# Kernel tuning notes

Hardware: AMD Instinct MI355X
Metric: run time of the kernel (lower is better)

Reference implementation:

```python
import jax, jax.numpy as jnp
import numpy as np

N = 128   # n_features == out_dim (required by the Christoffel permutes)
H = 256   # MLP hidden width of forward_func
B = 16    # batch size (state_batch is [2B, N])
EPS_G = 1e-4
EPS_DG = 1e-6
EPS_V = 1e-6


def setup_inputs() -> dict:
    key = jax.random.key(0)
    ks = jax.random.split(key, 6)
    return {
        "t": jax.random.uniform(ks[0], (), dtype=jnp.float32),
        "state_batch": jax.random.normal(ks[1], (2 * B, N), dtype=jnp.float32) * 0.1,
        "x0_batch": jax.random.normal(ks[2], (B, N), dtype=jnp.float32),
        "x1_batch": jax.random.normal(ks[3], (B, N), dtype=jnp.float32),
        "W1": jax.random.normal(ks[4], (N, H), dtype=jnp.float32) / np.float32(np.sqrt(N)),
        "b1": jnp.zeros((H,), dtype=jnp.float32),
        "W2": jax.random.normal(ks[5], (H, N), dtype=jnp.float32) / np.float32(np.sqrt(H)),
        "b2": jnp.zeros((N,), dtype=jnp.float32),
    }


def reference(t, state_batch, x0_batch, x1_batch, W1, b1, W2, b2):
    def f(x):  # forward_func, per-sample: [N] -> [N]
        return jnp.tanh(x @ W1 + b1) @ W2 + b2

    def metric(x):  # G(x) = J J^T + 1e-4 I, per-sample: [N] -> [N, N]
        J = jax.jacrev(f)(x)                      # [N, N], matches per-output grad loop
        return J @ J.T + EPS_G * jnp.eye(N, dtype=x.dtype)

    deviation, dev_velocity = jnp.split(state_batch, 2, axis=0)  # each [B, N]
    window = 4.0 * t * (1.0 - t)
    # x along the perturbed straight path
    x = x0_batch + t * (x1_batch - x0_batch) + window * deviation  # [B, N]

    # dG[b, i, j, k] = dG_ij/dx_k -- replaces the out_dim^2 autograd.grad loop
    dG = jax.vmap(jax.jacfwd(metric))(x)  # [B, N, N, N]
    nrm = jnp.sqrt(jnp.sum(dG * dG, axis=(1, 2, 3), keepdims=True))
    dG = dG / (nrm + EPS_DG)

    # Christoffel-like symbols
    Gamma = 0.5 * (dG + jnp.transpose(dG, (0, 2, 1, 3)) - jnp.transpose(dG, (0, 3, 1, 2)))
    a = -jnp.einsum('bijk,bj,bk->bi', Gamma, dev_velocity, dev_velocity)
    a = a / (jnp.linalg.norm(dev_velocity, axis=1, keepdims=True) + EPS_V)

    restoration = -0.1 * deviation
    return jnp.concatenate([dev_velocity, a + restoration], axis=0)  # [2B, N]
```

## Files before the change

kernel.cpp:

```cpp
#include <hip/hip_runtime.h>
#include <math.h>


static constexpr int OFF_W2T  = 0;
static constexpr int OFF_S    = 32768;
static constexpr int OFF_Q    = 98304;
static constexpr int OFF_D    = 163840;
static constexpr int OFF_C    = 167936;
static constexpr int OFF_UV   = 172032;
static constexpr int OFF_AV   = 176128;
static constexpr int OFF_VN   = 180224;
static constexpr int OFF_SUM  = 180240;
static constexpr int OFF_CNT  = 180256;
static constexpr int OFF_PT   = 180272;
static constexpr int OFF_PN   = OFF_PT + 16 * 32768;

__global__ __launch_bounds__(256) void k_stage1(const float* __restrict__ tptr,
                                                const float* __restrict__ state,
                                                const float* __restrict__ x0,
                                                const float* __restrict__ x1,
                                                const float* __restrict__ W1,
                                                const float* __restrict__ b1,
                                                const float* __restrict__ W2,
                                                float* __restrict__ ws,
                                                float* __restrict__ out) {
    __shared__ __align__(16) float smem[2 * 32 * 34];
    int blk = blockIdx.x;
    int tid = threadIdx.x;

    if (blk < 64) {
        float* Ai = smem;
        float* Aj = smem + 1088;
        int m0 = (blk >> 3) * 32, n0 = (blk & 7) * 32;
        int lx = tid & 31, lr = tid >> 5;
        int tx = tid & 15, ty = tid >> 4;
        float a00 = 0, a01 = 0, a10 = 0, a11 = 0;
        for (int kc = 0; kc < 128; kc += 32) {
            #pragma unroll
            for (int i = 0; i < 4; ++i) {
                int k = lr + 8 * i;
                Ai[k * 34 + lx] = W1[(kc + k) * 256 + m0 + lx];
                Aj[k * 34 + lx] = W1[(kc + k) * 256 + n0 + lx];
            }
            __syncthreads();
            #pragma unroll
            for (int k = 0; k < 32; ++k) {
                float2 a = *(const float2*)&Ai[k * 34 + 2 * ty];
                float2 b = *(const float2*)&Aj[k * 34 + 2 * tx];
                a00 += a.x * b.x; a01 += a.x * b.y;
                a10 += a.y * b.x; a11 += a.y * b.y;
            }
            __syncthreads();
        }
        float* S = ws + OFF_S;
        int m = m0 + 2 * ty, n = n0 + 2 * tx;
        S[m * 256 + n]           = a00;
        S[m * 256 + n + 1]       = a01;
        S[(m + 1) * 256 + n]     = a10;
        S[(m + 1) * 256 + n + 1] = a11;
    } else if (blk < 128) {
        float* Xi = smem;
        float* Xj = smem + 1088;
        int bq = blk - 64;
        int m0 = (bq >> 3) * 32, n0 = (bq & 7) * 32;
        int lx = tid & 31, lr = tid >> 5;
        int tx = tid & 15, ty = tid >> 4;
        float a00 = 0, a01 = 0, a10 = 0, a11 = 0;
        for (int kc = 0; kc < 128; kc += 32) {
            #pragma unroll
            for (int i = 0; i < 4; ++i) {
                Xi[lx * 34 + lr + 8 * i] = W2[(m0 + lr + 8 * i) * 128 + kc + lx];
                Xj[lx * 34 + lr + 8 * i] = W2[(n0 + lr + 8 * i) * 128 + kc + lx];
            }
            __syncthreads();
            #pragma unroll
            for (int k = 0; k < 32; ++k) {
                float2 a = *(const float2*)&Xi[k * 34 + 2 * ty];
                float2 b = *(const float2*)&Xj[k * 34 + 2 * tx];
                a00 += a.x * b.x; a01 += a.x * b.y;
                a10 += a.y * b.x; a11 += a.y * b.y;
            }
            __syncthreads();
        }
        float* Q = ws + OFF_Q;
        int m = m0 + 2 * ty, n = n0 + 2 * tx;
        Q[m * 256 + n]           = a00;
        Q[m * 256 + n + 1]       = a01;
        Q[(m + 1) * 256 + n]     = a10;
        Q[(m + 1) * 256 + n + 1] = a11;
    } else if (blk < 160) {
        float* tile = smem;
        int b2 = blk - 128;
        int c0 = (b2 & 3) * 32, r0 = (b2 >> 2) * 32;
        int tx = tid & 31, ty = tid >> 5;
        #pragma unroll
        for (int i = 0; i < 32; i += 8)
            tile[(ty + i) * 33 + tx] = W2[(r0 + ty + i) * 128 + c0 + tx];
        __syncthreads();
        float* W2T = ws + OFF_W2T;
        #pragma unroll
        for (int i = 0; i < 32; i += 8)
            W2T[(c0 + ty + i) * 256 + r0 + tx] = tile[tx * 33 + ty + i];
    } else {
        int b = blk - 160;
        float* xs  = smem;
        float* vs  = smem + 128;
        float* red = smem + 256;
        float t = tptr[0];
        float w = 4.f * t * (1.f - t);
        if (tid == 0) {
            ws[OFF_SUM + b] = 0.f;
            ((int*)(ws + OFF_CNT))[b] = 0;
        }
        if (tid < 128) {
            float dev = state[b * 128 + tid];
            float v   = state[(16 + b) * 128 + tid];
            float xv  = x0[b * 128 + tid] + t * (x1[b * 128 + tid] - x0[b * 128 + tid]) + w * dev;
            xs[tid] = xv;
            vs[tid] = v;
            out[b * 128 + tid] = v;
            red[tid] = v * v;
        }
        __syncthreads();
        for (int s = 64; s > 0; s >>= 1) {
            if (tid < s) red[tid] += red[tid + s];
            __syncthreads();
        }
        if (tid == 0) ws[OFF_VN + b] = sqrtf(red[0]);

        int m = tid;
        float h = b1[m], uvm = 0.f;
        #pragma unroll 8
        for (int k = 0; k < 128; ++k) {
            float wv = W1[k * 256 + m];
            h   += xs[k] * wv;
            uvm += vs[k] * wv;
        }
        float z  = tanhf(h);
        float dd = 1.f - z * z;
        float cc = -2.f * z * dd;
        const float4* w2r = (const float4*)&W2[m * 128];
        const float4* vs4 = (const float4*)vs;
        float avm = 0.f;
        #pragma unroll 8
        for (int j4 = 0; j4 < 32; ++j4) {
            float4 ww = w2r[j4];
            float4 vv = vs4[j4];
            avm += ww.x * vv.x + ww.y * vv.y + ww.z * vv.z + ww.w * vv.w;
        }
        ws[OFF_D  + b * 256 + m] = dd;
        ws[OFF_C  + b * 256 + m] = cc;
        ws[OFF_UV + b * 256 + m] = uvm;
        ws[OFF_AV + b * 256 + m] = avm;
    }
}

__global__ __launch_bounds__(256) void k_pmat3(const float* __restrict__ Smat,
                                               const float* __restrict__ dall,
                                               const float* __restrict__ W2,
                                               float* __restrict__ PT,
                                               float* __restrict__ Pn) {
    __shared__ __align__(16) float ST[32 * 36];
    __shared__ __align__(16) float YT[32 * 68];
    int b = blockIdx.z, mt = blockIdx.y, jt = blockIdx.x;
    int m0 = mt * 32, j0 = jt * 64;
    const float* dvec = dall + b * 256;
    int tid = threadIdx.x;
    int n = tid >> 3, c4 = (tid & 7) * 4;
    int ty = tid >> 5, tx = tid & 31;
    float acc[4][2] = {};
    for (int nc = 0; nc < 256; nc += 32) {
        *(float4*)&ST[n * 36 + c4] = *(const float4*)&Smat[(nc + n) * 256 + m0 + c4];
        float dn = dvec[nc + n];
        #pragma unroll
        for (int i = 0; i < 2; ++i) {
            int col = c4 + 32 * i;
            float4 wv = *(const float4*)&W2[(nc + n) * 128 + j0 + col];
            wv.x *= dn; wv.y *= dn; wv.z *= dn; wv.w *= dn;
            *(float4*)&YT[n * 68 + col] = wv;
        }
        __syncthreads();
        #pragma unroll 8
        for (int k = 0; k < 32; ++k) {
            float4 a  = *(const float4*)&ST[k * 36 + 4 * ty];
            float2 bb = *(const float2*)&YT[k * 68 + 2 * tx];
            acc[0][0] += a.x * bb.x; acc[0][1] += a.x * bb.y;
            acc[1][0] += a.y * bb.x; acc[1][1] += a.y * bb.y;
            acc[2][0] += a.z * bb.x; acc[2][1] += a.z * bb.y;
            acc[3][0] += a.w * bb.x; acc[3][1] += a.w * bb.y;
        }
        __syncthreads();
    }
    float* ptb = PT + b * 32768;
    float* pnb = Pn + b * 32768;
    #pragma unroll
    for (int jj = 0; jj < 2; ++jj) {
        float4 v = make_float4(acc[0][jj], acc[1][jj], acc[2][jj], acc[3][jj]);
        *(float4*)&ptb[(j0 + 2 * tx + jj) * 256 + m0 + 4 * ty] = v;
    }
    #pragma unroll
    for (int ii = 0; ii < 4; ++ii) {
        float2 v = make_float2(acc[ii][0], acc[ii][1]);
        *(float2*)&pnb[(m0 + 4 * ty + ii) * 128 + j0 + 2 * tx] = v;
    }
}

__global__ __launch_bounds__(256, 3) void k_fnorm6(const float* __restrict__ state,
                                                   const float* __restrict__ W2,
                                                   float* __restrict__ ws,
                                                   float* __restrict__ out) {
    __shared__ __align__(16) float lds[12544];
    int blk = blockIdx.x;
    int tid = threadIdx.x;
    int* cnt = (int*)(ws + OFF_CNT);

    if (blk < 16) {
        int b = blk;
        const float* ptb = ws + OFF_PT + b * 32768;
        const float* pnb = ws + OFF_PN + b * 32768;
        float* vs   = lds;
        float* g1   = lds + 128;
        float* g2   = lds + 384;
        float* red  = lds + 640;
        float* snrm = lds + 900;
        if (tid < 128) vs[tid] = state[(16 + b) * 128 + tid];
        __syncthreads();

        int m = tid;
        float pv = 0.f;
        #pragma unroll 8
        for (int j = 0; j < 128; ++j)
            pv += ptb[j * 256 + m] * vs[j];
        float cc  = ws[OFF_C  + b * 256 + m];
        float uvm = ws[OFF_UV + b * 256 + m];
        float avm = ws[OFF_AV + b * 256 + m];
        g1[m] = cc * pv  * uvm;
        g2[m] = cc * avm * uvm;
        __syncthreads();

        int i = tid & 127, half = tid >> 7;
        int mmlo = half * 128;
        float raw = 0.f;
        #pragma unroll 8
        for (int mm = mmlo; mm < mmlo + 128; ++mm)
            raw += W2[mm * 128 + i] * g1[mm] + pnb[mm * 128 + i] * g2[mm];
        red[tid] = raw;
        __syncthreads();

        if (tid == 0) {
            while (atomicAdd(&cnt[b], 0) < 36) __builtin_amdgcn_s_sleep(2);
            __threadfence();
            float tot = atomicAdd(&ws[OFF_SUM + b], 0.0f);
            snrm[0] = sqrtf(fmaxf(2.f * tot, 0.f));
        }
        __syncthreads();
        if (tid < 128) {
            float rawt = red[tid] + red[tid + 128];
            float vn = ws[OFF_VN + b];
            float a  = -0.5f * rawt / ((snrm[0] + 1e-6f) * (vn + 1e-6f));
            out[(16 + b) * 128 + tid] = a - 0.1f * state[b * 128 + tid];
        }
        return;
    }

    int q   = blk - 16;
    int idx = q >> 4;
    int b   = q & 15;
    int tj = 0;
    while ((tj + 1) * (tj + 2) / 2 <= idx) ++tj;
    int ti = idx - tj * (tj + 1) / 2;
    int mi0 = ti * 32, mj0 = tj * 32;
    float* PiT = lds;
    float* PjT = lds + 2048;
    float* WiT = lds + 4096;
    float* WjT = lds + 6144;
    const float* ptb = ws + OFF_PT + b * 32768;
    const float* W2T = ws + OFF_W2T;
    const float* Smat = ws + OFF_S;
    const float* Qmat = ws + OFF_Q;
    int jr = tid >> 3, jc4 = (tid & 7) * 4;
    int w = tid >> 6, s = tid & 63;
    int ty = s >> 3, tx = s & 7;
    float r[4][4] = {}, f[4][4] = {}, g[4][4] = {};
    #pragma unroll
    for (int rr = 0; rr < 2; ++rr) {
        #pragma unroll
        for (int it = 0; it < 2; ++it) {
            int l = jr + 32 * it;
            int j = 32 * (l >> 4) + 16 * rr + (l & 15);
            *(float4*)&PiT[l * 32 + jc4] = *(const float4*)&ptb[j * 256 + mi0 + jc4];
            *(float4*)&PjT[l * 32 + jc4] = *(const float4*)&ptb[j * 256 + mj0 + jc4];
            *(float4*)&WiT[l * 32 + jc4] = *(const float4*)&W2T[j * 256 + mi0 + jc4];
            *(float4*)&WjT[l * 32 + jc4] = *(const float4*)&W2T[j * 256 + mj0 + jc4];
        }
        __syncthreads();
        #pragma unroll 4
        for (int jj = 0; jj < 16; ++jj) {
            int l = 16 * w + jj;
            float4 pi4 = *(const float4*)&PiT[l * 32 + 4 * ty];
            float4 pj4 = *(const float4*)&PjT[l * 32 + 4 * tx];
            float4 wi4 = *(const float4*)&WiT[l * 32 + 4 * ty];
            float4 wj4 = *(const float4*)&WjT[l * 32 + 4 * tx];
            float pi[4] = {pi4.x, pi4.y, pi4.z, pi4.w};
            float pj[4] = {pj4.x, pj4.y, pj4.z, pj4.w};
            float wi[4] = {wi4.x, wi4.y, wi4.z, wi4.w};
            float wj[4] = {wj4.x, wj4.y, wj4.z, wj4.w};
            #pragma unroll
            for (int ii = 0; ii < 4; ++ii)
                #pragma unroll
                for (int kk = 0; kk < 4; ++kk) {
                    r[ii][kk] += pi[ii] * pj[kk];
                    f[ii][kk] += pi[ii] * wj[kk];
                    g[ii][kk] += pj[kk] * wi[ii];
                }
        }
        __syncthreads();
    }
    {
        float* scr = lds;
        int base = tid * 49;
        #pragma unroll
        for (int ii = 0; ii < 4; ++ii)
            #pragma unroll
            for (int kk = 0; kk < 4; ++kk) {
                scr[base + ii * 4 + kk]      = r[ii][kk];
                scr[base + 16 + ii * 4 + kk] = f[ii][kk];
                scr[base + 32 + ii * 4 + kk] = g[ii][kk];
            }
    }
    __syncthreads();
    if (tid < 64) {
        const float* scr = lds;
        float tr[16], tf[16], tg[16];
        #pragma unroll
        for (int k = 0; k < 16; ++k) {
            tr[k] = scr[tid * 49 + k]           + scr[(tid + 64) * 49 + k]
                  + scr[(tid + 128) * 49 + k]   + scr[(tid + 192) * 49 + k];
            tf[k] = scr[tid * 49 + 16 + k]      + scr[(tid + 64) * 49 + 16 + k]
                  + scr[(tid + 128) * 49 + 16 + k] + scr[(tid + 192) * 49 + 16 + k];
            tg[k] = scr[tid * 49 + 32 + k]      + scr[(tid + 64) * 49 + 32 + k]
                  + scr[(tid + 128) * 49 + 32 + k] + scr[(tid + 192) * 49 + 32 + k];
        }
        const float* cb = ws + OFF_C + b * 256;
        int mi = mi0 + 4 * (tid >> 3), mj = mj0 + 4 * (tid & 7);
        float4 ce4 = *(const float4*)&cb[mj];
        float ce[4] = {ce4.x, ce4.y, ce4.z, ce4.w};
        float sum = 0.f;
        #pragma unroll
        for (int ii = 0; ii < 4; ++ii) {
            float ci = cb[mi + ii];
            float4 S4 = *(const float4*)&Smat[(mi + ii) * 256 + mj];
            float4 Q4 = *(const float4*)&Qmat[(mi + ii) * 256 + mj];
            float Sv[4] = {S4.x, S4.y, S4.z, S4.w};
            float Qv[4] = {Q4.x, Q4.y, Q4.z, Q4.w};
            #pragma unroll
            for (int kk = 0; kk < 4; ++kk)
                sum += ci * ce[kk] * Sv[kk] * (Qv[kk] * tr[ii * 4 + kk] + tf[ii * 4 + kk] * tg[ii * 4 + kk]);
        }
        if (ti < tj) sum *= 2.f;
        #pragma unroll
        for (int off = 32; off > 0; off >>= 1)
            sum += __shfl_down(sum, off);
        if (tid == 0) {
            atomicAdd(&ws[OFF_SUM + b], sum);
            __threadfence();
            atomicAdd(&cnt[b], 1);
        }
    }
}

extern "C" void kernel_launch(void* const* d_in, const int* in_sizes, int n_in,
                              void* d_out, int out_size, void* d_ws, size_t ws_size,
                              hipStream_t stream) {
    (void)in_sizes; (void)n_in; (void)out_size; (void)ws_size;
    const float* t     = (const float*)d_in[0];
    const float* state = (const float*)d_in[1];
    const float* x0    = (const float*)d_in[2];
    const float* x1    = (const float*)d_in[3];
    const float* W1    = (const float*)d_in[4];
    const float* b1    = (const float*)d_in[5];
    const float* W2    = (const float*)d_in[6];
    float* out = (float*)d_out;
    float* ws  = (float*)d_ws;

    k_stage1<<<176, 256, 0, stream>>>(t, state, x0, x1, W1, b1, W2, ws, out);
    k_pmat3<<<dim3(2, 8, 16), 256, 0, stream>>>(ws + OFF_S, ws + OFF_D, W2,
                                                ws + OFF_PT, ws + OFF_PN);
    k_fnorm6<<<592, 256, 0, stream>>>(state, W2, ws, out);
}
```

Baseline: 115.0 us.

## Fuse three kernels into one persistent launch with inter-block flag dependencies

Merges the stage1, pmat3 and fnorm6 kernels into a single 976-block launch. Producer blocks signal completion with magic-number flags in workspace, and consumer blocks spin-wait on only the flags they depend on, which replaces the kernel boundaries with fine-grained dataflow. Some stage1 roles now process two tiles per block to cut the producer block count, and the final reduction reads one partial set from registers. This removes launch gaps and full-grid barriers, but relies on all producers being scheduled ahead of spinning consumers; stale magic values left in workspace from a previous call could also release waiters early.

```diff
diff --git a/kernel.cpp b/kernel.cpp
--- a/kernel.cpp
+++ b/kernel.cpp
@@ -12,10 +12,27 @@
 static constexpr int OFF_VN   = 180224;
 static constexpr int OFF_SUM  = 180240;
 static constexpr int OFF_CNT  = 180256;
-static constexpr int OFF_PT   = 180272;
+static constexpr int IFL_S    = 180272;
+static constexpr int IFL_Q    = IFL_S + 128;
+static constexpr int IFL_T    = IFL_Q + 64;
+static constexpr int IFL_PREP = IFL_T + 32;
+static constexpr int IFL_P    = IFL_PREP + 32;
+static constexpr int OFF_PT   = IFL_P + 512;
 static constexpr int OFF_PN   = OFF_PT + 16 * 32768;
 
-__global__ __launch_bounds__(256) void k_stage1(const float* __restrict__ tptr,
+#define MAG1 0x1357ACE5
+#define MAG2 0x2468BD1B
+
+__device__ __forceinline__ void set_flag2(int* f) {
+    atomicExch(f, MAG1);
+    atomicExch(f + 1, MAG2);
+}
+__device__ __forceinline__ void wait_flag2(int* f) {
+    while (atomicAdd(f, 0) != MAG1) __builtin_amdgcn_s_sleep(8);
+    while (atomicAdd(f + 1, 0) != MAG2) __builtin_amdgcn_s_sleep(8);
+}
+
+__global__ __launch_bounds__(256, 4) void k_all(const float* __restrict__ tptr,
                                                 const float* __restrict__ state,
                                                 const float* __restrict__ x0,
                                                 const float* __restrict__ x1,
@@ -24,13 +41,15 @@
                                                 const float* __restrict__ W2,
                                                 float* __restrict__ ws,
                                                 float* __restrict__ out) {
-    __shared__ __align__(16) float smem[2 * 32 * 34];
+    __shared__ __align__(16) float lds[9408];
     int blk = blockIdx.x;
     int tid = threadIdx.x;
+    int* flg = (int*)ws;
+    int* cnt = flg + OFF_CNT;
 
     if (blk < 64) {
-        float* Ai = smem;
-        float* Aj = smem + 1088;
+        float* Ai = lds;
+        float* Aj = lds + 1088;
         int m0 = (blk >> 3) * 32, n0 = (blk & 7) * 32;
         int lx = tid & 31, lr = tid >> 5;
         int tx = tid & 15, ty = tid >> 4;
@@ -58,59 +77,71 @@
         S[m * 256 + n + 1]       = a01;
         S[(m + 1) * 256 + n]     = a10;
         S[(m + 1) * 256 + n + 1] = a11;
+        __syncthreads();
+        if (tid == 0) { __threadfence(); set_flag2(flg + IFL_S + 2 * blk); }
+    } else if (blk < 96) {
+        int bqq = blk - 64;
+        for (int hh = 0; hh < 2; ++hh) {
+            int bq = bqq + 32 * hh;
+            float* Xi = lds;
+            float* Xj = lds + 1088;
+            int m0 = (bq >> 3) * 32, n0 = (bq & 7) * 32;
+            int lx = tid & 31, lr = tid >> 5;
+            int tx = tid & 15, ty = tid >> 4;
+            float a00 = 0, a01 = 0, a10 = 0, a11 = 0;
+            for (int kc = 0; kc < 128; kc += 32) {
+                #pragma unroll
+                for (int i = 0; i < 4; ++i) {
+                    Xi[lx * 34 + lr + 8 * i] = W2[(m0 + lr + 8 * i) * 128 + kc + lx];
+                    Xj[lx * 34 + lr + 8 * i] = W2[(n0 + lr + 8 * i) * 128 + kc + lx];
+                }
+                __syncthreads();
+                #pragma unroll
+                for (int k = 0; k < 32; ++k) {
+                    float2 a = *(const float2*)&Xi[k * 34 + 2 * ty];
+                    float2 b = *(const float2*)&Xj[k * 34 + 2 * tx];
+                    a00 += a.x * b.x; a01 += a.x * b.y;
+                    a10 += a.y * b.x; a11 += a.y * b.y;
+                }
+                __syncthreads();
+            }
+            float* Q = ws + OFF_Q;
+            int m = m0 + 2 * ty, n = n0 + 2 * tx;
+            Q[m * 256 + n]           = a00;
+            Q[m * 256 + n + 1]       = a01;
+            Q[(m + 1) * 256 + n]     = a10;
+            Q[(m + 1) * 256 + n + 1] = a11;
+            __syncthreads();
+        }
+        if (tid == 0) { __threadfence(); set_flag2(flg + IFL_Q + 2 * bqq); }
+    } else if (blk < 112) {
+        int bt = blk - 96;
+        for (int hh = 0; hh < 2; ++hh) {
+            int b2 = bt + 16 * hh;
+            float* tile = lds;
+            int c0 = (b2 & 3) * 32, r0 = (b2 >> 2) * 32;
+            int tx = tid & 31, ty = tid >> 5;
+            #pragma unroll
+            for (int i = 0; i < 32; i += 8)
+                tile[(ty + i) * 33 + tx] = W2[(r0 + ty + i) * 128 + c0 + tx];
+            __syncthreads();
+            float* W2T = ws + OFF_W2T;
+            #pragma unroll
+            for (int i = 0; i < 32; i += 8)
+                W2T[(c0 + ty + i) * 256 + r0 + tx] = tile[tx * 33 + ty + i];
+            __syncthreads();
+        }
+        if (tid == 0) { __threadfence(); set_flag2(flg + IFL_T + 2 * bt); }
     } else if (blk < 128) {
-        float* Xi = smem;
-        float* Xj = smem + 1088;
-        int bq = blk - 64;
-        int m0 = (bq >> 3) * 32, n0 = (bq & 7) * 32;
-        int lx = tid & 31, lr = tid >> 5;
-        int tx = tid & 15, ty = tid >> 4;
-        float a00 = 0, a01 = 0, a10 = 0, a11 = 0;
-        for (int kc = 0; kc < 128; kc += 32) {
-            #pragma unroll
-            for (int i = 0; i < 4; ++i) {
-                Xi[lx * 34 + lr + 8 * i] = W2[(m0 + lr + 8 * i) * 128 + kc + lx];
-                Xj[lx * 34 + lr + 8 * i] = W2[(n0 + lr + 8 * i) * 128 + kc + lx];
-            }
-            __syncthreads();
-            #pragma unroll
-            for (int k = 0; k < 32; ++k) {
-                float2 a = *(const float2*)&Xi[k * 34 + 2 * ty];
-                float2 b = *(const float2*)&Xj[k * 34 + 2 * tx];
-                a00 += a.x * b.x; a01 += a.x * b.y;
-                a10 += a.y * b.x; a11 += a.y * b.y;
-            }
-            __syncthreads();
-        }
-        float* Q = ws + OFF_Q;
-        int m = m0 + 2 * ty, n = n0 + 2 * tx;
-        Q[m * 256 + n]           = a00;
-        Q[m * 256 + n + 1]       = a01;
-        Q[(m + 1) * 256 + n]     = a10;
-        Q[(m + 1) * 256 + n + 1] = a11;
-    } else if (blk < 160) {
-        float* tile = smem;
-        int b2 = blk - 128;
-        int c0 = (b2 & 3) * 32, r0 = (b2 >> 2) * 32;
-        int tx = tid & 31, ty = tid >> 5;
-        #pragma unroll
-        for (int i = 0; i < 32; i += 8)
-            tile[(ty + i) * 33 + tx] = W2[(r0 + ty + i) * 128 + c0 + tx];
-        __syncthreads();
-        float* W2T = ws + OFF_W2T;
-        #pragma unroll
-        for (int i = 0; i < 32; i += 8)
-            W2T[(c0 + ty + i) * 256 + r0 + tx] = tile[tx * 33 + ty + i];
-    } else {
-        int b = blk - 160;
-        float* xs  = smem;
-        float* vs  = smem + 128;
-        float* red = smem + 256;
+        int b = blk - 112;
+        float* xs  = lds;
+        float* vs  = lds + 128;
+        float* red = lds + 256;
         float t = tptr[0];
         float w = 4.f * t * (1.f - t);
         if (tid == 0) {
             ws[OFF_SUM + b] = 0.f;
-            ((int*)(ws + OFF_CNT))[b] = 0;
+            cnt[b] = 0;
         }
         if (tid < 128) {
             float dev = state[b * 128 + tid];
@@ -152,70 +183,185 @@
         ws[OFF_C  + b * 256 + m] = cc;
         ws[OFF_UV + b * 256 + m] = uvm;
         ws[OFF_AV + b * 256 + m] = avm;
-    }
-}
-
-__global__ __launch_bounds__(256) void k_pmat3(const float* __restrict__ Smat,
-                                               const float* __restrict__ dall,
-                                               const float* __restrict__ W2,
-                                               float* __restrict__ PT,
-                                               float* __restrict__ Pn) {
-    __shared__ __align__(16) float ST[32 * 36];
-    __shared__ __align__(16) float YT[32 * 68];
-    int b = blockIdx.z, mt = blockIdx.y, jt = blockIdx.x;
-    int m0 = mt * 32, j0 = jt * 64;
-    const float* dvec = dall + b * 256;
-    int tid = threadIdx.x;
-    int n = tid >> 3, c4 = (tid & 7) * 4;
-    int ty = tid >> 5, tx = tid & 31;
-    float acc[4][2] = {};
-    for (int nc = 0; nc < 256; nc += 32) {
-        *(float4*)&ST[n * 36 + c4] = *(const float4*)&Smat[(nc + n) * 256 + m0 + c4];
-        float dn = dvec[nc + n];
+        __syncthreads();
+        if (tid == 0) { __threadfence(); set_flag2(flg + IFL_PREP + 2 * b); }
+    } else if (blk < 384) {
+        int q = blk - 128;
+        int b = q >> 4, rem = q & 15;
+        int mt = rem >> 1, jt = rem & 1;
+        if (tid < 64) wait_flag2(flg + IFL_S + 2 * tid);
+        else if (tid == 64) wait_flag2(flg + IFL_PREP + 2 * b);
+        __syncthreads();
+        __threadfence();
+
+        float* ST = lds;
+        float* YT = lds + 1152;
+        const float* Smat = ws + OFF_S;
+        const float* dvec = ws + OFF_D + b * 256;
+        int m0 = mt * 32, j0 = jt * 64;
+        int n = tid >> 3, c4 = (tid & 7) * 4;
+        int ty = tid >> 5, tx = tid & 31;
+        float acc[4][2] = {};
+        for (int nc = 0; nc < 256; nc += 32) {
+            *(float4*)&ST[n * 36 + c4] = *(const float4*)&Smat[(nc + n) * 256 + m0 + c4];
+            float dn = dvec[nc + n];
+            #pragma unroll
+            for (int i = 0; i < 2; ++i) {
+                int col = c4 + 32 * i;
+                float4 wv = *(const float4*)&W2[(nc + n) * 128 + j0 + col];
+                wv.x *= dn; wv.y *= dn; wv.z *= dn; wv.w *= dn;
+                *(float4*)&YT[n * 68 + col] = wv;
+            }
+            __syncthreads();
+            #pragma unroll 8
+            for (int k = 0; k < 32; ++k) {
+                float4 a  = *(const float4*)&ST[k * 36 + 4 * ty];
+                float2 bb = *(const float2*)&YT[k * 68 + 2 * tx];
+                acc[0][0] += a.x * bb.x; acc[0][1] += a.x * bb.y;
+                acc[1][0] += a.y * bb.x; acc[1][1] += a.y * bb.y;
+                acc[2][0] += a.z * bb.x; acc[2][1] += a.z * bb.y;
+                acc[3][0] += a.w * bb.x; acc[3][1] += a.w * bb.y;
+            }
+            __syncthreads();
+        }
+        float* ptb = ws + OFF_PT + b * 32768;
+        float* pnb = ws + OFF_PN + b * 32768;
         #pragma unroll
-        for (int i = 0; i < 2; ++i) {
-            int col = c4 + 32 * i;
-            float4 wv = *(const float4*)&W2[(nc + n) * 128 + j0 + col];
-            wv.x *= dn; wv.y *= dn; wv.z *= dn; wv.w *= dn;
-            *(float4*)&YT[n * 68 + col] = wv;
-        }
-        __syncthreads();
-        #pragma unroll 8
-        for (int k = 0; k < 32; ++k) {
-            float4 a  = *(const float4*)&ST[k * 36 + 4 * ty];
-            float2 bb = *(const float2*)&YT[k * 68 + 2 * tx];
-            acc[0][0] += a.x * bb.x; acc[0][1] += a.x * bb.y;
-            acc[1][0] += a.y * bb.x; acc[1][1] += a.y * bb.y;
-            acc[2][0] += a.z * bb.x; acc[2][1] += a.z * bb.y;
-            acc[3][0] += a.w * bb.x; acc[3][1] += a.w * bb.y;
-        }
-        __syncthreads();
-    }
-    float* ptb = PT + b * 32768;
-    float* pnb = Pn + b * 32768;
-    #pragma unroll
-    for (int jj = 0; jj < 2; ++jj) {
-        float4 v = make_float4(acc[0][jj], acc[1][jj], acc[2][jj], acc[3][jj]);
-        *(float4*)&ptb[(j0 + 2 * tx + jj) * 256 + m0 + 4 * ty] = v;
-    }
-    #pragma unroll
-    for (int ii = 0; ii < 4; ++ii) {
-        float2 v = make_float2(acc[ii][0], acc[ii][1]);
-        *(float2*)&pnb[(m0 + 4 * ty + ii) * 128 + j0 + 2 * tx] = v;
-    }
-}
-
-__global__ __launch_bounds__(256, 3) void k_fnorm6(const float* __restrict__ state,
-                                                   const float* __restrict__ W2,
-                                                   float* __restrict__ ws,
-                                                   float* __restrict__ out) {
-    __shared__ __align__(16) float lds[12544];
-    int blk = blockIdx.x;
-    int tid = threadIdx.x;
-    int* cnt = (int*)(ws + OFF_CNT);
-
-    if (blk < 16) {
-        int b = blk;
+        for (int jj = 0; jj < 2; ++jj) {
+            float4 v = make_float4(acc[0][jj], acc[1][jj], acc[2][jj], acc[3][jj]);
+            *(float4*)&ptb[(j0 + 2 * tx + jj) * 256 + m0 + 4 * ty] = v;
+        }
+        #pragma unroll
+        for (int ii = 0; ii < 4; ++ii) {
+            float2 v = make_float2(acc[ii][0], acc[ii][1]);
+            *(float2*)&pnb[(m0 + 4 * ty + ii) * 128 + j0 + 2 * tx] = v;
+        }
+        __syncthreads();
+        if (tid == 0) { __threadfence(); set_flag2(flg + IFL_P + 2 * q); }
+    } else if (blk < 960) {
+        int q = blk - 384;
+        int idx = q >> 4;
+        int b   = q & 15;
+        if (tid < 16) wait_flag2(flg + IFL_P + 2 * (16 * b + tid));
+        else if (tid < 48) wait_flag2(flg + IFL_Q + 2 * (tid - 16));
+        else if (tid < 64) wait_flag2(flg + IFL_T + 2 * (tid - 48));
+        __syncthreads();
+        __threadfence();
+
+        int tj = 0;
+        while ((tj + 1) * (tj + 2) / 2 <= idx) ++tj;
+        int ti = idx - tj * (tj + 1) / 2;
+        int mi0 = ti * 32, mj0 = tj * 32;
+        float* PiT = lds;
+        float* PjT = lds + 2048;
+        float* WiT = lds + 4096;
+        float* WjT = lds + 6144;
+        const float* ptb  = ws + OFF_PT + b * 32768;
+        const float* W2T  = ws + OFF_W2T;
+        const float* Smat = ws + OFF_S;
+        const float* Qmat = ws + OFF_Q;
+        int jr = tid >> 3, jc4 = (tid & 7) * 4;
+        int w = tid >> 6, s = tid & 63;
+        int ty = s >> 3, tx = s & 7;
+        float r[4][4] = {}, f[4][4] = {}, g[4][4] = {};
+        #pragma unroll
+        for (int rr = 0; rr < 2; ++rr) {
+            #pragma unroll
+            for (int it = 0; it < 2; ++it) {
+                int l = jr + 32 * it;
+                int j = 32 * (l >> 4) + 16 * rr + (l & 15);
+                *(float4*)&PiT[l * 32 + jc4] = *(const float4*)&ptb[j * 256 + mi0 + jc4];
+                *(float4*)&PjT[l * 32 + jc4] = *(const float4*)&ptb[j * 256 + mj0 + jc4];
+                *(float4*)&WiT[l * 32 + jc4] = *(const float4*)&W2T[j * 256 + mi0 + jc4];
+                *(float4*)&WjT[l * 32 + jc4] = *(const float4*)&W2T[j * 256 + mj0 + jc4];
+            }
+            __syncthreads();
+            #pragma unroll 4
+            for (int jj = 0; jj < 16; ++jj) {
+                int l = 16 * w + jj;
+                float4 pi4 = *(const float4*)&PiT[l * 32 + 4 * ty];
+                float4 pj4 = *(const float4*)&PjT[l * 32 + 4 * tx];
+                float4 wi4 = *(const float4*)&WiT[l * 32 + 4 * ty];
+                float4 wj4 = *(const float4*)&WjT[l * 32 + 4 * tx];
+                float pi[4] = {pi4.x, pi4.y, pi4.z, pi4.w};
+                float pj[4] = {pj4.x, pj4.y, pj4.z, pj4.w};
+                float wi[4] = {wi4.x, wi4.y, wi4.z, wi4.w};
+                float wj[4] = {wj4.x, wj4.y, wj4.z, wj4.w};
+                #pragma unroll
+                for (int ii = 0; ii < 4; ++ii)
+                    #pragma unroll
+                    for (int kk = 0; kk < 4; ++kk) {
+                        r[ii][kk] += pi[ii] * pj[kk];
+                        f[ii][kk] += pi[ii] * wj[kk];
+                        g[ii][kk] += pj[kk] * wi[ii];
+                    }
+            }
+            __syncthreads();
+        }
+        if (w != 0) {
+            float* scr = lds;
+            int base = ((w - 1) * 64 + s) * 49;
+            #pragma unroll
+            for (int ii = 0; ii < 4; ++ii)
+                #pragma unroll
+                for (int kk = 0; kk < 4; ++kk) {
+                    scr[base + ii * 4 + kk]      = r[ii][kk];
+                    scr[base + 16 + ii * 4 + kk] = f[ii][kk];
+                    scr[base + 32 + ii * 4 + kk] = g[ii][kk];
+                }
+        }
+        __syncthreads();
+        if (tid < 64) {
+            float tr[16], tf[16], tg[16];
+            #pragma unroll
+            for (int ii = 0; ii < 4; ++ii)
+                #pragma unroll
+                for (int kk = 0; kk < 4; ++kk) {
+                    tr[ii * 4 + kk] = r[ii][kk];
+                    tf[ii * 4 + kk] = f[ii][kk];
+                    tg[ii * 4 + kk] = g[ii][kk];
+                }
+            for (int ww = 0; ww < 3; ++ww) {
+                const float* sc = lds + (ww * 64 + tid) * 49;
+                #pragma unroll
+                for (int k = 0; k < 16; ++k) {
+                    tr[k] += sc[k];
+                    tf[k] += sc[16 + k];
+                    tg[k] += sc[32 + k];
+                }
+            }
+            const float* cb = ws + OFF_C + b * 256;
+            int mi = mi0 + 4 * (tid >> 3), mj = mj0 + 4 * (tid & 7);
+            float4 ce4 = *(const float4*)&cb[mj];
+            float ce[4] = {ce4.x, ce4.y, ce4.z, ce4.w};
+            float sum = 0.f;
+            #pragma unroll
+            for (int ii = 0; ii < 4; ++ii) {
+                float ci = cb[mi + ii];
+                float4 S4 = *(const float4*)&Smat[(mi + ii) * 256 + mj];
+                float4 Q4 = *(const float4*)&Qmat[(mi + ii) * 256 + mj];
+                float Sv[4] = {S4.x, S4.y, S4.z, S4.w};
+                float Qv[4] = {Q4.x, Q4.y, Q4.z, Q4.w};
+                #pragma unroll
+                for (int kk = 0; kk < 4; ++kk)
+                    sum += ci * ce[kk] * Sv[kk] * (Qv[kk] * tr[ii * 4 + kk] + tf[ii * 4 + kk] * tg[ii * 4 + kk]);
+            }
+            if (ti < tj) sum *= 2.f;
+            #pragma unroll
+            for (int off = 32; off > 0; off >>= 1)
+                sum += __shfl_down(sum, off);
+            if (tid == 0) {
+                atomicAdd(&ws[OFF_SUM + b], sum);
+                __threadfence();
+                atomicAdd(&cnt[b], 1);
+            }
+        }
+    } else {
+        int b = blk - 960;
+        if (tid < 16) wait_flag2(flg + IFL_P + 2 * (16 * b + tid));
+        __syncthreads();
+        __threadfence();
+
         const float* ptb = ws + OFF_PT + b * 32768;
         const float* pnb = ws + OFF_PN + b * 32768;
         float* vs   = lds;
@@ -248,7 +394,7 @@
         __syncthreads();
 
         if (tid == 0) {
-            while (atomicAdd(&cnt[b], 0) < 36) __builtin_amdgcn_s_sleep(2);
+            while (atomicAdd(&cnt[b], 0) < 36) __builtin_amdgcn_s_sleep(8);
             __threadfence();
             float tot = atomicAdd(&ws[OFF_SUM + b], 0.0f);
             snrm[0] = sqrtf(fmaxf(2.f * tot, 0.f));
@@ -259,112 +405,6 @@
             float vn = ws[OFF_VN + b];
             float a  = -0.5f * rawt / ((snrm[0] + 1e-6f) * (vn + 1e-6f));
             out[(16 + b) * 128 + tid] = a - 0.1f * state[b * 128 + tid];
-        }
-        return;
-    }
-
-    int q   = blk - 16;
-    int idx = q >> 4;
-    int b   = q & 15;
-    int tj = 0;
-    while ((tj + 1) * (tj + 2) / 2 <= idx) ++tj;
-    int ti = idx - tj * (tj + 1) / 2;
-    int mi0 = ti * 32, mj0 = tj * 32;
-    float* PiT = lds;
-    float* PjT = lds + 2048;
-    float* WiT = lds + 4096;
-    float* WjT = lds + 6144;
-    const float* ptb = ws + OFF_PT + b * 32768;
-    const float* W2T = ws + OFF_W2T;
-    const float* Smat = ws + OFF_S;
-    const float* Qmat = ws + OFF_Q;
-    int jr = tid >> 3, jc4 = (tid & 7) * 4;
-    int w = tid >> 6, s = tid & 63;
-    int ty = s >> 3, tx = s & 7;
-    float r[4][4] = {}, f[4][4] = {}, g[4][4] = {};
-    #pragma unroll
-    for (int rr = 0; rr < 2; ++rr) {
-        #pragma unroll
-        for (int it = 0; it < 2; ++it) {
-            int l = jr + 32 * it;
-            int j = 32 * (l >> 4) + 16 * rr + (l & 15);
-            *(float4*)&PiT[l * 32 + jc4] = *(const float4*)&ptb[j * 256 + mi0 + jc4];
-            *(float4*)&PjT[l * 32 + jc4] = *(const float4*)&ptb[j * 256 + mj0 + jc4];
-            *(float4*)&WiT[l * 32 + jc4] = *(const float4*)&W2T[j * 256 + mi0 + jc4];
-            *(float4*)&WjT[l * 32 + jc4] = *(const float4*)&W2T[j * 256 + mj0 + jc4];
-        }
-        __syncthreads();
-        #pragma unroll 4
-        for (int jj = 0; jj < 16; ++jj) {
-            int l = 16 * w + jj;
-            float4 pi4 = *(const float4*)&PiT[l * 32 + 4 * ty];
-            float4 pj4 = *(const float4*)&PjT[l * 32 + 4 * tx];
-            float4 wi4 = *(const float4*)&WiT[l * 32 + 4 * ty];
-            float4 wj4 = *(const float4*)&WjT[l * 32 + 4 * tx];
-            float pi[4] = {pi4.x, pi4.y, pi4.z, pi4.w};
-            float pj[4] = {pj4.x, pj4.y, pj4.z, pj4.w};
-            float wi[4] = {wi4.x, wi4.y, wi4.z, wi4.w};
-            float wj[4] = {wj4.x, wj4.y, wj4.z, wj4.w};
-            #pragma unroll
-            for (int ii = 0; ii < 4; ++ii)
-                #pragma unroll
-                for (int kk = 0; kk < 4; ++kk) {
-                    r[ii][kk] += pi[ii] * pj[kk];
-                    f[ii][kk] += pi[ii] * wj[kk];
-                    g[ii][kk] += pj[kk] * wi[ii];
-                }
-        }
-        __syncthreads();
-    }
-    {
-        float* scr = lds;
-        int base = tid * 49;
-        #pragma unroll
-        for (int ii = 0; ii < 4; ++ii)
-            #pragma unroll
-            for (int kk = 0; kk < 4; ++kk) {
-                scr[base + ii * 4 + kk]      = r[ii][kk];
-                scr[base + 16 + ii * 4 + kk] = f[ii][kk];
-                scr[base + 32 + ii * 4 + kk] = g[ii][kk];
-            }
-    }
-    __syncthreads();
-    if (tid < 64) {
-        const float* scr = lds;
-        float tr[16], tf[16], tg[16];
-        #pragma unroll
-        for (int k = 0; k < 16; ++k) {
-            tr[k] = scr[tid * 49 + k]           + scr[(tid + 64) * 49 + k]
-                  + scr[(tid + 128) * 49 + k]   + scr[(tid + 192) * 49 + k];
-            tf[k] = scr[tid * 49 + 16 + k]      + scr[(tid + 64) * 49 + 16 + k]
-                  + scr[(tid + 128) * 49 + 16 + k] + scr[(tid + 192) * 49 + 16 + k];
-            tg[k] = scr[tid * 49 + 32 + k]      + scr[(tid + 64) * 49 + 32 + k]
-                  + scr[(tid + 128) * 49 + 32 + k] + scr[(tid + 192) * 49 + 32 + k];
-        }
-        const float* cb = ws + OFF_C + b * 256;
-        int mi = mi0 + 4 * (tid >> 3), mj = mj0 + 4 * (tid & 7);
-        float4 ce4 = *(const float4*)&cb[mj];
-        float ce[4] = {ce4.x, ce4.y, ce4.z, ce4.w};
-        float sum = 0.f;
-        #pragma unroll
-        for (int ii = 0; ii < 4; ++ii) {
-            float ci = cb[mi + ii];
-            float4 S4 = *(const float4*)&Smat[(mi + ii) * 256 + mj];
-            float4 Q4 = *(const float4*)&Qmat[(mi + ii) * 256 + mj];
-            float Sv[4] = {S4.x, S4.y, S4.z, S4.w};
-            float Qv[4] = {Q4.x, Q4.y, Q4.z, Q4.w};
-            #pragma unroll
-            for (int kk = 0; kk < 4; ++kk)
-                sum += ci * ce[kk] * Sv[kk] * (Qv[kk] * tr[ii * 4 + kk] + tf[ii * 4 + kk] * tg[ii * 4 + kk]);
-        }
-        if (ti < tj) sum *= 2.f;
-        #pragma unroll
-        for (int off = 32; off > 0; off >>= 1)
-            sum += __shfl_down(sum, off);
-        if (tid == 0) {
-            atomicAdd(&ws[OFF_SUM + b], sum);
-            __threadfence();
-            atomicAdd(&cnt[b], 1);
         }
     }
 }
@@ -383,8 +423,5 @@
     float* out = (float*)d_out;
     float* ws  = (float*)d_ws;
 
-    k_stage1<<<176, 256, 0, stream>>>(t, state, x0, x1, W1, b1, W2, ws, out);
-    k_pmat3<<<dim3(2, 8, 16), 256, 0, stream>>>(ws + OFF_S, ws + OFF_D, W2,
-                                                ws + OFF_PT, ws + OFF_PN);
-    k_fnorm6<<<592, 256, 0, stream>>>(state, W2, ws, out);
+    k_all<<<976, 256, 0, stream>>>(t, state, x0, x1, W1, b1, W2, ws, out);
 }
```

Measured after the change: 206.8 us. 79.8% more time.

## Fuse P-matrix GEMM into the norm kernel with per-batch counter handoff

Applied to the files above, without the earlier changes.

Merges the P-matrix GEMM kernel and the norm/output kernel into one launch of 848 blocks. The first 256 blocks compute PT/Pn and signal per-batch completion through a new counter. The norm-tile and final-output blocks spin-wait on that counter instead of relying on a kernel boundary, which removes one launch and lets batches proceed independently. The block order is rearranged so the output blocks come last, and the cross-wave reduction keeps wave 0's partials in registers, which cuts LDS use and allows occupancy 4. The cost is spin-wait deadlock risk if the consumer blocks become resident before the producers, plus sleep/poll overhead.

```diff
diff --git a/kernel.cpp b/kernel.cpp
--- a/kernel.cpp
+++ b/kernel.cpp
@@ -12,7 +12,8 @@
 static constexpr int OFF_VN   = 180224;
 static constexpr int OFF_SUM  = 180240;
 static constexpr int OFF_CNT  = 180256;
-static constexpr int OFF_PT   = 180272;
+static constexpr int OFF_CNT2 = 180272;
+static constexpr int OFF_PT   = 180288;
 static constexpr int OFF_PN   = OFF_PT + 16 * 32768;
 
 __global__ __launch_bounds__(256) void k_stage1(const float* __restrict__ tptr,
@@ -110,7 +111,8 @@
         float w = 4.f * t * (1.f - t);
         if (tid == 0) {
             ws[OFF_SUM + b] = 0.f;
-            ((int*)(ws + OFF_CNT))[b] = 0;
+            ((int*)ws)[OFF_CNT + b]  = 0;
+            ((int*)ws)[OFF_CNT2 + b] = 0;
         }
         if (tid < 128) {
             float dev = state[b * 128 + tid];
@@ -155,67 +157,190 @@
     }
 }
 
-__global__ __launch_bounds__(256) void k_pmat3(const float* __restrict__ Smat,
-                                               const float* __restrict__ dall,
-                                               const float* __restrict__ W2,
-                                               float* __restrict__ PT,
-                                               float* __restrict__ Pn) {
-    __shared__ __align__(16) float ST[32 * 36];
-    __shared__ __align__(16) float YT[32 * 68];
-    int b = blockIdx.z, mt = blockIdx.y, jt = blockIdx.x;
-    int m0 = mt * 32, j0 = jt * 64;
-    const float* dvec = dall + b * 256;
-    int tid = threadIdx.x;
-    int n = tid >> 3, c4 = (tid & 7) * 4;
-    int ty = tid >> 5, tx = tid & 31;
-    float acc[4][2] = {};
-    for (int nc = 0; nc < 256; nc += 32) {
-        *(float4*)&ST[n * 36 + c4] = *(const float4*)&Smat[(nc + n) * 256 + m0 + c4];
-        float dn = dvec[nc + n];
-        #pragma unroll
-        for (int i = 0; i < 2; ++i) {
-            int col = c4 + 32 * i;
-            float4 wv = *(const float4*)&W2[(nc + n) * 128 + j0 + col];
-            wv.x *= dn; wv.y *= dn; wv.z *= dn; wv.w *= dn;
-            *(float4*)&YT[n * 68 + col] = wv;
-        }
-        __syncthreads();
-        #pragma unroll 8
-        for (int k = 0; k < 32; ++k) {
-            float4 a  = *(const float4*)&ST[k * 36 + 4 * ty];
-            float2 bb = *(const float2*)&YT[k * 68 + 2 * tx];
-            acc[0][0] += a.x * bb.x; acc[0][1] += a.x * bb.y;
-            acc[1][0] += a.y * bb.x; acc[1][1] += a.y * bb.y;
-            acc[2][0] += a.z * bb.x; acc[2][1] += a.z * bb.y;
-            acc[3][0] += a.w * bb.x; acc[3][1] += a.w * bb.y;
-        }
-        __syncthreads();
-    }
-    float* ptb = PT + b * 32768;
-    float* pnb = Pn + b * 32768;
-    #pragma unroll
-    for (int jj = 0; jj < 2; ++jj) {
-        float4 v = make_float4(acc[0][jj], acc[1][jj], acc[2][jj], acc[3][jj]);
-        *(float4*)&ptb[(j0 + 2 * tx + jj) * 256 + m0 + 4 * ty] = v;
-    }
-    #pragma unroll
-    for (int ii = 0; ii < 4; ++ii) {
-        float2 v = make_float2(acc[ii][0], acc[ii][1]);
-        *(float2*)&pnb[(m0 + 4 * ty + ii) * 128 + j0 + 2 * tx] = v;
-    }
-}
-
-__global__ __launch_bounds__(256, 3) void k_fnorm6(const float* __restrict__ state,
-                                                   const float* __restrict__ W2,
-                                                   float* __restrict__ ws,
-                                                   float* __restrict__ out) {
-    __shared__ __align__(16) float lds[12544];
+__global__ __launch_bounds__(256, 4) void k_pfuse(const float* __restrict__ state,
+                                                  const float* __restrict__ W2,
+                                                  float* __restrict__ ws,
+                                                  float* __restrict__ out) {
+    __shared__ __align__(16) float lds[9408];
     int blk = blockIdx.x;
     int tid = threadIdx.x;
-    int* cnt = (int*)(ws + OFF_CNT);
-
-    if (blk < 16) {
-        int b = blk;
+    int* cnt  = (int*)ws + OFF_CNT;
+    int* cnt2 = (int*)ws + OFF_CNT2;
+
+    if (blk < 256) {
+        int q = blk;
+        int b = q >> 4, rem = q & 15;
+        int mt = rem >> 1, jt = rem & 1;
+        float* ST = lds;
+        float* YT = lds + 1152;
+        const float* Smat = ws + OFF_S;
+        const float* dvec = ws + OFF_D + b * 256;
+        int m0 = mt * 32, j0 = jt * 64;
+        int n = tid >> 3, c4 = (tid & 7) * 4;
+        int ty = tid >> 5, tx = tid & 31;
+        float acc[4][2] = {};
+        for (int nc = 0; nc < 256; nc += 32) {
+            *(float4*)&ST[n * 36 + c4] = *(const float4*)&Smat[(nc + n) * 256 + m0 + c4];
+            float dn = dvec[nc + n];
+            #pragma unroll
+            for (int i = 0; i < 2; ++i) {
+                int col = c4 + 32 * i;
+                float4 wv = *(const float4*)&W2[(nc + n) * 128 + j0 + col];
+                wv.x *= dn; wv.y *= dn; wv.z *= dn; wv.w *= dn;
+                *(float4*)&YT[n * 68 + col] = wv;
+            }
+            __syncthreads();
+            #pragma unroll 8
+            for (int k = 0; k < 32; ++k) {
+                float4 a  = *(const float4*)&ST[k * 36 + 4 * ty];
+                float2 bb = *(const float2*)&YT[k * 68 + 2 * tx];
+                acc[0][0] += a.x * bb.x; acc[0][1] += a.x * bb.y;
+                acc[1][0] += a.y * bb.x; acc[1][1] += a.y * bb.y;
+                acc[2][0] += a.z * bb.x; acc[2][1] += a.z * bb.y;
+                acc[3][0] += a.w * bb.x; acc[3][1] += a.w * bb.y;
+            }
+            __syncthreads();
+        }
+        float* ptb = ws + OFF_PT + b * 32768;
+        float* pnb = ws + OFF_PN + b * 32768;
+        #pragma unroll
+        for (int jj = 0; jj < 2; ++jj) {
+            float4 v = make_float4(acc[0][jj], acc[1][jj], acc[2][jj], acc[3][jj]);
+            *(float4*)&ptb[(j0 + 2 * tx + jj) * 256 + m0 + 4 * ty] = v;
+        }
+        #pragma unroll
+        for (int ii = 0; ii < 4; ++ii) {
+            float2 v = make_float2(acc[ii][0], acc[ii][1]);
+            *(float2*)&pnb[(m0 + 4 * ty + ii) * 128 + j0 + 2 * tx] = v;
+        }
+        __syncthreads();
+        if (tid == 0) { __threadfence(); atomicAdd(&cnt2[b], 1); }
+    } else if (blk < 832) {
+        int q = blk - 256;
+        int idx = q >> 4;
+        int b   = q & 15;
+        if (tid == 0) {
+            while (atomicAdd(&cnt2[b], 0) < 16) __builtin_amdgcn_s_sleep(4);
+            __threadfence();
+        }
+        __syncthreads();
+
+        int tj = 0;
+        while ((tj + 1) * (tj + 2) / 2 <= idx) ++tj;
+        int ti = idx - tj * (tj + 1) / 2;
+        int mi0 = ti * 32, mj0 = tj * 32;
+        float* PiT = lds;
+        float* PjT = lds + 2048;
+        float* WiT = lds + 4096;
+        float* WjT = lds + 6144;
+        const float* ptb  = ws + OFF_PT + b * 32768;
+        const float* W2T  = ws + OFF_W2T;
+        const float* Smat = ws + OFF_S;
+        const float* Qmat = ws + OFF_Q;
+        int jr = tid >> 3, jc4 = (tid & 7) * 4;
+        int w = tid >> 6, s = tid & 63;
+        int ty = s >> 3, tx = s & 7;
+        float r[4][4] = {}, f[4][4] = {}, g[4][4] = {};
+        #pragma unroll
+        for (int rr = 0; rr < 2; ++rr) {
+            #pragma unroll
+            for (int it = 0; it < 2; ++it) {
+                int l = jr + 32 * it;
+                int j = 32 * (l >> 4) + 16 * rr + (l & 15);
+                *(float4*)&PiT[l * 32 + jc4] = *(const float4*)&ptb[j * 256 + mi0 + jc4];
+                *(float4*)&PjT[l * 32 + jc4] = *(const float4*)&ptb[j * 256 + mj0 + jc4];
+                *(float4*)&WiT[l * 32 + jc4] = *(const float4*)&W2T[j * 256 + mi0 + jc4];
+                *(float4*)&WjT[l * 32 + jc4] = *(const float4*)&W2T[j * 256 + mj0 + jc4];
+            }
+            __syncthreads();
+            #pragma unroll 4
+            for (int jj = 0; jj < 16; ++jj) {
+                int l = 16 * w + jj;
+                float4 pi4 = *(const float4*)&PiT[l * 32 + 4 * ty];
+                float4 pj4 = *(const float4*)&PjT[l * 32 + 4 * tx];
+                float4 wi4 = *(const float4*)&WiT[l * 32 + 4 * ty];
+                float4 wj4 = *(const float4*)&WjT[l * 32 + 4 * tx];
+                float pi[4] = {pi4.x, pi4.y, pi4.z, pi4.w};
+                float pj[4] = {pj4.x, pj4.y, pj4.z, pj4.w};
+                float wi[4] = {wi4.x, wi4.y, wi4.z, wi4.w};
+                float wj[4] = {wj4.x, wj4.y, wj4.z, wj4.w};
+                #pragma unroll
+                for (int ii = 0; ii < 4; ++ii)
+                    #pragma unroll
+                    for (int kk = 0; kk < 4; ++kk) {
+                        r[ii][kk] += pi[ii] * pj[kk];
+                        f[ii][kk] += pi[ii] * wj[kk];
+                        g[ii][kk] += pj[kk] * wi[ii];
+                    }
+            }
+            __syncthreads();
+        }
+        if (w != 0) {
+            float* scr = lds;
+            int base = ((w - 1) * 64 + s) * 49;
+            #pragma unroll
+            for (int ii = 0; ii < 4; ++ii)
+                #pragma unroll
+                for (int kk = 0; kk < 4; ++kk) {
+                    scr[base + ii * 4 + kk]      = r[ii][kk];
+                    scr[base + 16 + ii * 4 + kk] = f[ii][kk];
+                    scr[base + 32 + ii * 4 + kk] = g[ii][kk];
+                }
+        }
+        __syncthreads();
+        if (tid < 64) {
+            float tr[16], tf[16], tg[16];
+            #pragma unroll
+            for (int ii = 0; ii < 4; ++ii)
+                #pragma unroll
+                for (int kk = 0; kk < 4; ++kk) {
+                    tr[ii * 4 + kk] = r[ii][kk];
+                    tf[ii * 4 + kk] = f[ii][kk];
+                    tg[ii * 4 + kk] = g[ii][kk];
+                }
+            for (int ww = 0; ww < 3; ++ww) {
+                const float* sc = lds + (ww * 64 + tid) * 49;
+                #pragma unroll
+                for (int k = 0; k < 16; ++k) {
+                    tr[k] += sc[k];
+                    tf[k] += sc[16 + k];
+                    tg[k] += sc[32 + k];
+                }
+            }
+            const float* cb = ws + OFF_C + b * 256;
+            int mi = mi0 + 4 * (tid >> 3), mj = mj0 + 4 * (tid & 7);
+            float4 ce4 = *(const float4*)&cb[mj];
+            float ce[4] = {ce4.x, ce4.y, ce4.z, ce4.w};
+            float sum = 0.f;
+            #pragma unroll
+            for (int ii = 0; ii < 4; ++ii) {
+                float ci = cb[mi + ii];
+                float4 S4 = *(const float4*)&Smat[(mi + ii) * 256 + mj];
+                float4 Q4 = *(const float4*)&Qmat[(mi + ii) * 256 + mj];
+                float Sv[4] = {S4.x, S4.y, S4.z, S4.w};
+                float Qv[4] = {Q4.x, Q4.y, Q4.z, Q4.w};
+                #pragma unroll
+                for (int kk = 0; kk < 4; ++kk)
+                    sum += ci * ce[kk] * Sv[kk] * (Qv[kk] * tr[ii * 4 + kk] + tf[ii * 4 + kk] * tg[ii * 4 + kk]);
+            }
+            if (ti < tj) sum *= 2.f;
+            #pragma unroll
+            for (int off = 32; off > 0; off >>= 1)
+                sum += __shfl_down(sum, off);
+            if (tid == 0) {
+                atomicAdd(&ws[OFF_SUM + b], sum);
+                __threadfence();
+                atomicAdd(&cnt[b], 1);
+            }
+        }
+    } else {
+        int b = blk - 832;
+        if (tid == 0) {
+            while (atomicAdd(&cnt2[b], 0) < 16) __builtin_amdgcn_s_sleep(4);
+            __threadfence();
+        }
+        __syncthreads();
+
         const float* ptb = ws + OFF_PT + b * 32768;
         const float* pnb = ws + OFF_PN + b * 32768;
         float* vs   = lds;
@@ -248,7 +373,7 @@
         __syncthreads();
 
         if (tid == 0) {
-            while (atomicAdd(&cnt[b], 0) < 36) __builtin_amdgcn_s_sleep(2);
+            while (atomicAdd(&cnt[b], 0) < 36) __builtin_amdgcn_s_sleep(4);
             __threadfence();
             float tot = atomicAdd(&ws[OFF_SUM + b], 0.0f);
             snrm[0] = sqrtf(fmaxf(2.f * tot, 0.f));
@@ -259,112 +384,6 @@
             float vn = ws[OFF_VN + b];
             float a  = -0.5f * rawt / ((snrm[0] + 1e-6f) * (vn + 1e-6f));
             out[(16 + b) * 128 + tid] = a - 0.1f * state[b * 128 + tid];
-        }
-        return;
-    }
-
-    int q   = blk - 16;
-    int idx = q >> 4;
-    int b   = q & 15;
-    int tj = 0;
-    while ((tj + 1) * (tj + 2) / 2 <= idx) ++tj;
-    int ti = idx - tj * (tj + 1) / 2;
-    int mi0 = ti * 32, mj0 = tj * 32;
-    float* PiT = lds;
-    float* PjT = lds + 2048;
-    float* WiT = lds + 4096;
-    float* WjT = lds + 6144;
-    const float* ptb = ws + OFF_PT + b * 32768;
-    const float* W2T = ws + OFF_W2T;
-    const float* Smat = ws + OFF_S;
-    const float* Qmat = ws + OFF_Q;
-    int jr = tid >> 3, jc4 = (tid & 7) * 4;
-    int w = tid >> 6, s = tid & 63;
-    int ty = s >> 3, tx = s & 7;
-    float r[4][4] = {}, f[4][4] = {}, g[4][4] = {};
-    #pragma unroll
-    for (int rr = 0; rr < 2; ++rr) {
-        #pragma unroll
-        for (int it = 0; it < 2; ++it) {
-            int l = jr + 32 * it;
-            int j = 32 * (l >> 4) + 16 * rr + (l & 15);
-            *(float4*)&PiT[l * 32 + jc4] = *(const float4*)&ptb[j * 256 + mi0 + jc4];
-            *(float4*)&PjT[l * 32 + jc4] = *(const float4*)&ptb[j * 256 + mj0 + jc4];
-            *(float4*)&WiT[l * 32 + jc4] = *(const float4*)&W2T[j * 256 + mi0 + jc4];
-            *(float4*)&WjT[l * 32 + jc4] = *(const float4*)&W2T[j * 256 + mj0 + jc4];
-        }
-        __syncthreads();
-        #pragma unroll 4
-        for (int jj = 0; jj < 16; ++jj) {
-            int l = 16 * w + jj;
-            float4 pi4 = *(const float4*)&PiT[l * 32 + 4 * ty];
-            float4 pj4 = *(const float4*)&PjT[l * 32 + 4 * tx];
-            float4 wi4 = *(const float4*)&WiT[l * 32 + 4 * ty];
-            float4 wj4 = *(const float4*)&WjT[l * 32 + 4 * tx];
-            float pi[4] = {pi4.x, pi4.y, pi4.z, pi4.w};
-            float pj[4] = {pj4.x, pj4.y, pj4.z, pj4.w};
-            float wi[4] = {wi4.x, wi4.y, wi4.z, wi4.w};
-            float wj[4] = {wj4.x, wj4.y, wj4.z, wj4.w};
-            #pragma unroll
-            for (int ii = 0; ii < 4; ++ii)
-                #pragma unroll
-                for (int kk = 0; kk < 4; ++kk) {
-                    r[ii][kk] += pi[ii] * pj[kk];
-                    f[ii][kk] += pi[ii] * wj[kk];
-                    g[ii][kk] += pj[kk] * wi[ii];
-                }
-        }
-        __syncthreads();
-    }
-    {
-        float* scr = lds;
-        int base = tid * 49;
-        #pragma unroll
-        for (int ii = 0; ii < 4; ++ii)
-            #pragma unroll
-            for (int kk = 0; kk < 4; ++kk) {
-                scr[base + ii * 4 + kk]      = r[ii][kk];
-                scr[base + 16 + ii * 4 + kk] = f[ii][kk];
-                scr[base + 32 + ii * 4 + kk] = g[ii][kk];
-            }
-    }
-    __syncthreads();
-    if (tid < 64) {
-        const float* scr = lds;
-        float tr[16], tf[16], tg[16];
-        #pragma unroll
-        for (int k = 0; k < 16; ++k) {
-            tr[k] = scr[tid * 49 + k]           + scr[(tid + 64) * 49 + k]
-                  + scr[(tid + 128) * 49 + k]   + scr[(tid + 192) * 49 + k];
-            tf[k] = scr[tid * 49 + 16 + k]      + scr[(tid + 64) * 49 + 16 + k]
-                  + scr[(tid + 128) * 49 + 16 + k] + scr[(tid + 192) * 49 + 16 + k];
-            tg[k] = scr[tid * 49 + 32 + k]      + scr[(tid + 64) * 49 + 32 + k]
-                  + scr[(tid + 128) * 49 + 32 + k] + scr[(tid + 192) * 49 + 32 + k];
-        }
-        const float* cb = ws + OFF_C + b * 256;
-        int mi = mi0 + 4 * (tid >> 3), mj = mj0 + 4 * (tid & 7);
-        float4 ce4 = *(const float4*)&cb[mj];
-        float ce[4] = {ce4.x, ce4.y, ce4.z, ce4.w};
-        float sum = 0.f;
-        #pragma unroll
-        for (int ii = 0; ii < 4; ++ii) {
-            float ci = cb[mi + ii];
-            float4 S4 = *(const float4*)&Smat[(mi + ii) * 256 + mj];
-            float4 Q4 = *(const float4*)&Qmat[(mi + ii) * 256 + mj];
-            float Sv[4] = {S4.x, S4.y, S4.z, S4.w};
-            float Qv[4] = {Q4.x, Q4.y, Q4.z, Q4.w};
-            #pragma unroll
-            for (int kk = 0; kk < 4; ++kk)
-                sum += ci * ce[kk] * Sv[kk] * (Qv[kk] * tr[ii * 4 + kk] + tf[ii * 4 + kk] * tg[ii * 4 + kk]);
-        }
-        if (ti < tj) sum *= 2.f;
-        #pragma unroll
-        for (int off = 32; off > 0; off >>= 1)
-            sum += __shfl_down(sum, off);
-        if (tid == 0) {
-            atomicAdd(&ws[OFF_SUM + b], sum);
-            __threadfence();
-            atomicAdd(&cnt[b], 1);
         }
     }
 }
@@ -384,7 +403,5 @@
     float* ws  = (float*)d_ws;
 
     k_stage1<<<176, 256, 0, stream>>>(t, state, x0, x1, W1, b1, W2, ws, out);
-    k_pmat3<<<dim3(2, 8, 16), 256, 0, stream>>>(ws + OFF_S, ws + OFF_D, W2,
-                                                ws + OFF_PT, ws + OFF_PN);
-    k_fnorm6<<<592, 256, 0, stream>>>(state, W2, ws, out);
+    k_pfuse<<<848, 256, 0, stream>>>(state, W2, ws, out);
 }
```

Measured after the change: 149.8 us. +30.2%, slower.
